# Kernel tuning notes

Hardware: AMD Instinct MI355X
Metric: run time of the kernel (lower is better)

## Reference

```python
import jax, jax.numpy as jnp
import numpy as np
import math

# Module config (matches init_kwargs)
FILTERS = 128
OUT_FACTOR = 0.5
B, H, W, C = 64, 64, 64, 64
HC = int(math.ceil(H / 2))  # weight/crop height = 32
WC = int(math.ceil(W / 2))  # weight/crop width  = 32
R_MIN = int(math.ceil(H * (1 - OUT_FACTOR) / 2))  # 16
R_MAX = R_MIN + int(math.ceil(H * (1 - OUT_FACTOR)))  # 48
C_MIN = int(math.ceil(W * (1 - OUT_FACTOR) / 2))  # 16
C_MAX = C_MIN + int(math.ceil(W * (1 - OUT_FACTOR)))  # 48


def setup_inputs() -> dict:
    key = jax.random.key(0)
    k1, k2, k3 = jax.random.split(key, 3)
    x = jax.random.normal(k1, (B, 2, H, W, C), dtype=jnp.float32)
    # keras 'random_normal' initializer: stddev 0.05
    W_r = jax.random.normal(k2, (HC, WC, C, FILTERS), dtype=jnp.float32) * 0.05
    W_i = jax.random.normal(k3, (HC, WC, C, FILTERS), dtype=jnp.float32) * 0.05
    b_r = jnp.zeros((FILTERS,), dtype=jnp.float32)
    b_i = jnp.zeros((FILTERS,), dtype=jnp.float32)
    return {"x": x, "W_r": W_r, "W_i": W_i, "b_r": b_r, "b_i": b_i}


def reference(x, W_r, W_i, b_r, b_i):
    # Crop center region: (B, 2, HC, WC, C)
    sp = x[:, :, R_MIN:R_MAX, C_MIN:C_MAX, :]
    xr, xi = sp[:, 0], sp[:, 1]  # (B, HC, WC, C)
    # Locally-connected complex contraction over channels (per-pixel weights)
    rr = jnp.einsum('bhwc,hwcf->bhwf', xr, W_r)
    ii = jnp.einsum('bhwc,hwcf->bhwf', xi, W_i)
    ri = jnp.einsum('bhwc,hwcf->bhwf', xr, W_i)
    ir = jnp.einsum('bhwc,hwcf->bhwf', xi, W_r)
    r = rr - ii + b_r  # (B, HC, WC, F)
    i = ri + ir + b_i
    y = jnp.stack([r, i], axis=1)  # (B, 2, HC, WC, F)
    # CReLU: relu applied independently to real and imaginary parts
    return jax.nn.relu(y)
```

## Files before the change

kernel.cpp:

```cpp
#include <hip/hip_runtime.h>

typedef __attribute__((ext_vector_type(8))) short short8;
typedef __attribute__((ext_vector_type(4))) float f32x4;
typedef __attribute__((ext_vector_type(4))) unsigned u32x4;

#define XSTR 72

__device__ __forceinline__ unsigned f2bf(float f) {
    unsigned u = __float_as_uint(f);
    return (u + 0x7fffu + ((u >> 16) & 1u)) >> 16;
}
__device__ __forceinline__ unsigned pack2(float lo, float hi) {
    return f2bf(lo) | (f2bf(hi) << 16);
}

__global__ __launch_bounds__(256, 4) void cplx_dot_kernel(
    const float* __restrict__ x, const float* __restrict__ Wr,
    const float* __restrict__ Wi, const float* __restrict__ br,
    const float* __restrict__ bi, float* __restrict__ out)
{
    __shared__ __align__(16) short sWr[128 * XSTR];
    __shared__ __align__(16) short sWi[128 * XSTR];

    const int bid = blockIdx.x;
    const int h = bid >> 5, w = bid & 31;
    const int t = threadIdx.x;
    const int wv = t >> 6, l = t & 63;
    const int lr = l & 15, lh = l >> 4;

    const int brow = 16 * wv + lr;
    const size_t gx = ((((size_t)brow * 2) * 64 + (16 + h)) * 64 + (16 + w)) * 64;
    const size_t gimg = (size_t)64 * 64 * 64;

    f32x4 vr[2][2], vi[2][2];
    #pragma unroll
    for (int kk = 0; kk < 2; ++kk) {
        const int c0 = 32 * kk + 8 * lh;
        vr[kk][0] = *(const f32x4*)(x + gx + c0);
        vr[kk][1] = *(const f32x4*)(x + gx + c0 + 4);
        vi[kk][0] = *(const f32x4*)(x + gx + gimg + c0);
        vi[kk][1] = *(const f32x4*)(x + gx + gimg + c0 + 4);
    }
    u32x4 ar[2], ai[2];
    #pragma unroll
    for (int kk = 0; kk < 2; ++kk) {
        #pragma unroll
        for (int p = 0; p < 2; ++p) {
            ar[kk][2 * p]     = pack2(vr[kk][p][0], vr[kk][p][1]);
            ar[kk][2 * p + 1] = pack2(vr[kk][p][2], vr[kk][p][3]);
            ai[kk][2 * p]     = pack2(vi[kk][p][0], vi[kk][p][1]);
            ai[kk][2 * p + 1] = pack2(vi[kk][p][2], vi[kk][p][3]);
        }
    }

    {
        const int g = t & 31, cg = t >> 5;
        const size_t wbase = (((size_t)h * 32 + w) * 64) * 128;
        f32x4 rr[8], ri[8];
        #pragma unroll
        for (int i = 0; i < 8; ++i) {
            size_t off = wbase + (size_t)(8 * cg + i) * 128 + 4 * g;
            rr[i] = *(const f32x4*)(Wr + off);
            ri[i] = *(const f32x4*)(Wi + off);
        }
        #pragma unroll
        for (int j = 0; j < 4; ++j) {
            u32x4 pr, pi;
            pr[0] = pack2(rr[0][j], rr[1][j]); pr[1] = pack2(rr[2][j], rr[3][j]);
            pr[2] = pack2(rr[4][j], rr[5][j]); pr[3] = pack2(rr[6][j], rr[7][j]);
            pi[0] = pack2(ri[0][j], ri[1][j]); pi[1] = pack2(ri[2][j], ri[3][j]);
            pi[2] = pack2(ri[4][j], ri[5][j]); pi[3] = pack2(ri[6][j], ri[7][j]);
            *(u32x4*)&sWr[(4 * g + j) * XSTR + 8 * cg] = pr;
            *(u32x4*)&sWi[(4 * g + j) * XSTR + 8 * cg] = pi;
        }
    }
    __syncthreads();

    f32x4 accR[8], accI[8];
    #pragma unroll
    for (int ft = 0; ft < 8; ++ft) {
        #pragma unroll
        for (int j = 0; j < 4; ++j) { accR[ft][j] = 0.f; accI[ft][j] = 0.f; }
    }

    #pragma unroll
    for (int kk = 0; kk < 2; ++kk) {
        const int c0 = 32 * kk + 8 * lh;
        short8 arf = __builtin_bit_cast(short8, ar[kk]);
        short8 aif = __builtin_bit_cast(short8, ai[kk]);
        short8 anf;
        #pragma unroll
        for (int j = 0; j < 8; ++j) anf[j] = aif[j] ^ (short)0x8000;
        #pragma unroll
        for (int ft = 0; ft < 8; ++ft) {
            short8 wr_ = *(const short8*)&sWr[(16 * ft + lr) * XSTR + c0];
            short8 wi_ = *(const short8*)&sWi[(16 * ft + lr) * XSTR + c0];
            accR[ft] = __builtin_amdgcn_mfma_f32_16x16x32_bf16(arf, wr_, accR[ft], 0, 0, 0);
            accR[ft] = __builtin_amdgcn_mfma_f32_16x16x32_bf16(anf, wi_, accR[ft], 0, 0, 0);
            accI[ft] = __builtin_amdgcn_mfma_f32_16x16x32_bf16(arf, wi_, accI[ft], 0, 0, 0);
            accI[ft] = __builtin_amdgcn_mfma_f32_16x16x32_bf16(aif, wr_, accI[ft], 0, 0, 0);
        }
    }

    #pragma unroll
    for (int ft = 0; ft < 8; ++ft) {
        const int fc = 16 * ft + lr;
        const float vbr = br[fc], vbi = bi[fc];
        #pragma unroll
        for (int j = 0; j < 4; ++j) {
            const int b = 16 * wv + 4 * lh + j;
            size_t o = ((((size_t)b * 2) * 32 + h) * 32 + w) * 128 + fc;
            out[o] = fmaxf(accR[ft][j] + vbr, 0.f);
            out[o + (size_t)32 * 32 * 128] = fmaxf(accI[ft][j] + vbi, 0.f);
        }
    }
}

extern "C" void kernel_launch(void* const* d_in, const int* in_sizes, int n_in,
                              void* d_out, int out_size, void* d_ws, size_t ws_size,
                              hipStream_t stream) {
    const float* x  = (const float*)d_in[0];
    const float* Wr = (const float*)d_in[1];
    const float* Wi = (const float*)d_in[2];
    const float* br = (const float*)d_in[3];
    const float* bi = (const float*)d_in[4];
    float* out = (float*)d_out;
    hipLaunchKernelGGL(cplx_dot_kernel, dim3(1024), dim3(256), 0, stream,
                       x, Wr, Wi, br, bi, out);
}
```

Before: 30.70 us.

## Process two pixels per block with double-buffered weight staging and prefetch

Each block now handles two adjacent w positions. It prefetches the second pixel's x and weight data from global memory while the first pixel's MFMA work and stores run, using two LDS buffers. The grid is halved to 512 blocks and launch bounds are lowered to 2 blocks per SM. This is meant to hide global load latency behind compute, at the cost of more registers, double the LDS, and fewer blocks for the GPU's many CUs.

```diff
diff --git a/kernel.cpp b/kernel.cpp
--- a/kernel.cpp
+++ b/kernel.cpp
@@ -14,25 +14,12 @@
     return f2bf(lo) | (f2bf(hi) << 16);
 }
 
-__global__ __launch_bounds__(256, 4) void cplx_dot_kernel(
-    const float* __restrict__ x, const float* __restrict__ Wr,
-    const float* __restrict__ Wi, const float* __restrict__ br,
-    const float* __restrict__ bi, float* __restrict__ out)
-{
-    __shared__ __align__(16) short sWr[128 * XSTR];
-    __shared__ __align__(16) short sWi[128 * XSTR];
 
-    const int bid = blockIdx.x;
-    const int h = bid >> 5, w = bid & 31;
-    const int t = threadIdx.x;
-    const int wv = t >> 6, l = t & 63;
-    const int lr = l & 15, lh = l >> 4;
-
-    const int brow = 16 * wv + lr;
+__device__ __forceinline__ void load_x(const float* __restrict__ x, int brow,
+                                       int h, int w, int lh,
+                                       f32x4 vr[2][2], f32x4 vi[2][2]) {
     const size_t gx = ((((size_t)brow * 2) * 64 + (16 + h)) * 64 + (16 + w)) * 64;
     const size_t gimg = (size_t)64 * 64 * 64;
-
-    f32x4 vr[2][2], vi[2][2];
     #pragma unroll
     for (int kk = 0; kk < 2; ++kk) {
         const int c0 = 32 * kk + 8 * lh;
@@ -41,9 +28,12 @@
         vi[kk][0] = *(const f32x4*)(x + gx + gimg + c0);
         vi[kk][1] = *(const f32x4*)(x + gx + gimg + c0 + 4);
     }
-    u32x4 ar[2], ai[2];
+}
+
+__device__ __forceinline__ void pack_x(const f32x4 vr[2][2], const f32x4 vi[2][2],
+                                       u32x4 ar[2], u32x4 ai[2]) {
     #pragma unroll
-    for (int kk = 0; kk < 2; ++kk) {
+    for (int kk = 0; kk < 2; ++kk)
         #pragma unroll
         for (int p = 0; p < 2; ++p) {
             ar[kk][2 * p]     = pack2(vr[kk][p][0], vr[kk][p][1]);
@@ -51,38 +41,45 @@
             ai[kk][2 * p]     = pack2(vi[kk][p][0], vi[kk][p][1]);
             ai[kk][2 * p + 1] = pack2(vi[kk][p][2], vi[kk][p][3]);
         }
+}
+
+__device__ __forceinline__ void load_W(const float* __restrict__ Wr,
+                                       const float* __restrict__ Wi,
+                                       int h, int w, int g, int cg,
+                                       f32x4 rr[8], f32x4 ri[8]) {
+    const size_t wbase = (((size_t)h * 32 + w) * 64) * 128;
+    #pragma unroll
+    for (int i = 0; i < 8; ++i) {
+        size_t off = wbase + (size_t)(8 * cg + i) * 128 + 4 * g;
+        rr[i] = *(const f32x4*)(Wr + off);
+        ri[i] = *(const f32x4*)(Wi + off);
     }
+}
 
-    {
-        const int g = t & 31, cg = t >> 5;
-        const size_t wbase = (((size_t)h * 32 + w) * 64) * 128;
-        f32x4 rr[8], ri[8];
-        #pragma unroll
-        for (int i = 0; i < 8; ++i) {
-            size_t off = wbase + (size_t)(8 * cg + i) * 128 + 4 * g;
-            rr[i] = *(const f32x4*)(Wr + off);
-            ri[i] = *(const f32x4*)(Wi + off);
-        }
-        #pragma unroll
-        for (int j = 0; j < 4; ++j) {
-            u32x4 pr, pi;
-            pr[0] = pack2(rr[0][j], rr[1][j]); pr[1] = pack2(rr[2][j], rr[3][j]);
-            pr[2] = pack2(rr[4][j], rr[5][j]); pr[3] = pack2(rr[6][j], rr[7][j]);
-            pi[0] = pack2(ri[0][j], ri[1][j]); pi[1] = pack2(ri[2][j], ri[3][j]);
-            pi[2] = pack2(ri[4][j], ri[5][j]); pi[3] = pack2(ri[6][j], ri[7][j]);
-            *(u32x4*)&sWr[(4 * g + j) * XSTR + 8 * cg] = pr;
-            *(u32x4*)&sWi[(4 * g + j) * XSTR + 8 * cg] = pi;
-        }
+__device__ __forceinline__ void pack_W(short* __restrict__ sWr, short* __restrict__ sWi,
+                                       int g, int cg,
+                                       const f32x4 rr[8], const f32x4 ri[8]) {
+    #pragma unroll
+    for (int j = 0; j < 4; ++j) {
+        u32x4 pr, pi;
+        pr[0] = pack2(rr[0][j], rr[1][j]); pr[1] = pack2(rr[2][j], rr[3][j]);
+        pr[2] = pack2(rr[4][j], rr[5][j]); pr[3] = pack2(rr[6][j], rr[7][j]);
+        pi[0] = pack2(ri[0][j], ri[1][j]); pi[1] = pack2(ri[2][j], ri[3][j]);
+        pi[2] = pack2(ri[4][j], ri[5][j]); pi[3] = pack2(ri[6][j], ri[7][j]);
+        *(u32x4*)&sWr[(4 * g + j) * XSTR + 8 * cg] = pr;
+        *(u32x4*)&sWi[(4 * g + j) * XSTR + 8 * cg] = pi;
     }
-    __syncthreads();
+}
 
-    f32x4 accR[8], accI[8];
+__device__ __forceinline__ void compute(const short* __restrict__ sWr,
+                                        const short* __restrict__ sWi,
+                                        const u32x4 ar[2], const u32x4 ai[2],
+                                        int lr, int lh,
+                                        f32x4 accR[8], f32x4 accI[8]) {
     #pragma unroll
-    for (int ft = 0; ft < 8; ++ft) {
+    for (int ft = 0; ft < 8; ++ft)
         #pragma unroll
         for (int j = 0; j < 4; ++j) { accR[ft][j] = 0.f; accI[ft][j] = 0.f; }
-    }
-
     #pragma unroll
     for (int kk = 0; kk < 2; ++kk) {
         const int c0 = 32 * kk + 8 * lh;
@@ -101,19 +98,70 @@
             accI[ft] = __builtin_amdgcn_mfma_f32_16x16x32_bf16(aif, wr_, accI[ft], 0, 0, 0);
         }
     }
+}
 
+__device__ __forceinline__ void store_out(float* __restrict__ out,
+                                          const f32x4 accR[8], const f32x4 accI[8],
+                                          const float vbr[8], const float vbi[8],
+                                          int h, int w, int wv, int lr, int lh) {
     #pragma unroll
     for (int ft = 0; ft < 8; ++ft) {
         const int fc = 16 * ft + lr;
-        const float vbr = br[fc], vbi = bi[fc];
         #pragma unroll
         for (int j = 0; j < 4; ++j) {
             const int b = 16 * wv + 4 * lh + j;
             size_t o = ((((size_t)b * 2) * 32 + h) * 32 + w) * 128 + fc;
-            out[o] = fmaxf(accR[ft][j] + vbr, 0.f);
-            out[o + (size_t)32 * 32 * 128] = fmaxf(accI[ft][j] + vbi, 0.f);
+            out[o] = fmaxf(accR[ft][j] + vbr[ft], 0.f);
+            out[o + (size_t)32 * 32 * 128] = fmaxf(accI[ft][j] + vbi[ft], 0.f);
         }
     }
+}
+
+__global__ __launch_bounds__(256, 2) void cplx_dot_kernel(
+    const float* __restrict__ x, const float* __restrict__ Wr,
+    const float* __restrict__ Wi, const float* __restrict__ br,
+    const float* __restrict__ bi, float* __restrict__ out)
+{
+    __shared__ __align__(16) short sW[2][2][128 * XSTR];
+
+    const int bid = blockIdx.x;
+    const int h = bid >> 4, qw = bid & 15;
+    const int w0 = 2 * qw, w1 = 2 * qw + 1;
+    const int t = threadIdx.x;
+    const int wv = t >> 6, l = t & 63;
+    const int lr = l & 15, lh = l >> 4;
+    const int g = t & 31, cg = t >> 5;
+    const int brow = 16 * wv + lr;
+
+    float vbr[8], vbi[8];
+    #pragma unroll
+    for (int ft = 0; ft < 8; ++ft) { vbr[ft] = br[16 * ft + lr]; vbi[ft] = bi[16 * ft + lr]; }
+
+    f32x4 xr0[2][2], xi0[2][2];
+    load_x(x, brow, h, w0, lh, xr0, xi0);
+    f32x4 wr0[8], wi0[8];
+    load_W(Wr, Wi, h, w0, g, cg, wr0, wi0);
+    pack_W(&sW[0][0][0], &sW[0][1][0], g, cg, wr0, wi0);
+    u32x4 ar0[2], ai0[2];
+    pack_x(xr0, xi0, ar0, ai0);
+    __syncthreads();
+
+    f32x4 xr1[2][2], xi1[2][2];
+    load_x(x, brow, h, w1, lh, xr1, xi1);
+    f32x4 wr1[8], wi1[8];
+    load_W(Wr, Wi, h, w1, g, cg, wr1, wi1);
+
+    f32x4 accR[8], accI[8];
+    compute(&sW[0][0][0], &sW[0][1][0], ar0, ai0, lr, lh, accR, accI);
+    store_out(out, accR, accI, vbr, vbi, h, w0, wv, lr, lh);
+
+    pack_W(&sW[1][0][0], &sW[1][1][0], g, cg, wr1, wi1);
+    u32x4 ar1[2], ai1[2];
+    pack_x(xr1, xi1, ar1, ai1);
+    __syncthreads();
+
+    compute(&sW[1][0][0], &sW[1][1][0], ar1, ai1, lr, lh, accR, accI);
+    store_out(out, accR, accI, vbr, vbi, h, w1, wv, lr, lh);
 }
 
 extern "C" void kernel_launch(void* const* d_in, const int* in_sizes, int n_in,
@@ -125,6 +173,6 @@
     const float* br = (const float*)d_in[3];
     const float* bi = (const float*)d_in[4];
     float* out = (float*)d_out;
-    hipLaunchKernelGGL(cplx_dot_kernel, dim3(1024), dim3(256), 0, stream,
+    hipLaunchKernelGGL(cplx_dot_kernel, dim3(512), dim3(256), 0, stream,
                        x, Wr, Wi, br, bi, out);
 }
```

Result: slower. 31.64 us (+3.1%).

## Switch to 32x32x16 MFMA tiles with wave split over batch and filter halves

Applied to the files above, without the earlier changes.

Replaces the 16x16x32 bf16 MFMA tiling, where each wave handled 16 batch rows across all 128 filters, with 32x32x16 MFMAs. Each wave now covers 32 batch rows by 64 filters, so each wave reads half as much weight data from LDS. Output stores become nontemporal and the occupancy hint drops from 4 to 3 blocks per CU. The x operand conversion moves after the weight staging, and the accumulators are consumed per filter tile, which may lower register pressure but changes the order of the output writes.

```diff
diff --git a/kernel.cpp b/kernel.cpp
--- a/kernel.cpp
+++ b/kernel.cpp
@@ -2,6 +2,7 @@
 
 typedef __attribute__((ext_vector_type(8))) short short8;
 typedef __attribute__((ext_vector_type(4))) float f32x4;
+typedef __attribute__((ext_vector_type(16))) float f32x16;
 typedef __attribute__((ext_vector_type(4))) unsigned u32x4;
 
 #define XSTR 72
@@ -14,7 +15,7 @@
     return f2bf(lo) | (f2bf(hi) << 16);
 }
 
-__global__ __launch_bounds__(256, 4) void cplx_dot_kernel(
+__global__ __launch_bounds__(256, 3) void cplx_dot_kernel(
     const float* __restrict__ x, const float* __restrict__ Wr,
     const float* __restrict__ Wi, const float* __restrict__ br,
     const float* __restrict__ bi, float* __restrict__ out)
@@ -26,31 +27,22 @@
     const int h = bid >> 5, w = bid & 31;
     const int t = threadIdx.x;
     const int wv = t >> 6, l = t & 63;
-    const int lr = l & 15, lh = l >> 4;
+    const int m = l & 31, kb = l >> 5;
+    const int mt = wv >> 1, fhalf = wv & 1;
 
-    const int brow = 16 * wv + lr;
+    const size_t gimg = (size_t)64 * 64 * 64;
+    const size_t oimg = (size_t)32 * 32 * 128;
+
+    const int brow = 32 * mt + m;
     const size_t gx = ((((size_t)brow * 2) * 64 + (16 + h)) * 64 + (16 + w)) * 64;
-    const size_t gimg = (size_t)64 * 64 * 64;
-
-    f32x4 vr[2][2], vi[2][2];
+    f32x4 vr[4][2], vi[4][2];
     #pragma unroll
-    for (int kk = 0; kk < 2; ++kk) {
-        const int c0 = 32 * kk + 8 * lh;
+    for (int kk = 0; kk < 4; ++kk) {
+        const int c0 = 16 * kk + 8 * kb;
         vr[kk][0] = *(const f32x4*)(x + gx + c0);
         vr[kk][1] = *(const f32x4*)(x + gx + c0 + 4);
         vi[kk][0] = *(const f32x4*)(x + gx + gimg + c0);
         vi[kk][1] = *(const f32x4*)(x + gx + gimg + c0 + 4);
-    }
-    u32x4 ar[2], ai[2];
-    #pragma unroll
-    for (int kk = 0; kk < 2; ++kk) {
-        #pragma unroll
-        for (int p = 0; p < 2; ++p) {
-            ar[kk][2 * p]     = pack2(vr[kk][p][0], vr[kk][p][1]);
-            ar[kk][2 * p + 1] = pack2(vr[kk][p][2], vr[kk][p][3]);
-            ai[kk][2 * p]     = pack2(vi[kk][p][0], vi[kk][p][1]);
-            ai[kk][2 * p + 1] = pack2(vi[kk][p][2], vi[kk][p][3]);
-        }
     }
 
     {
@@ -74,44 +66,47 @@
             *(u32x4*)&sWi[(4 * g + j) * XSTR + 8 * cg] = pi;
         }
     }
+
+    short8 ar[4], ai[4], an[4];
+    #pragma unroll
+    for (int kk = 0; kk < 4; ++kk) {
+        u32x4 pr, pi;
+        #pragma unroll
+        for (int p = 0; p < 2; ++p) {
+            pr[2 * p]     = pack2(vr[kk][p][0], vr[kk][p][1]);
+            pr[2 * p + 1] = pack2(vr[kk][p][2], vr[kk][p][3]);
+            pi[2 * p]     = pack2(vi[kk][p][0], vi[kk][p][1]);
+            pi[2 * p + 1] = pack2(vi[kk][p][2], vi[kk][p][3]);
+        }
+        ar[kk] = __builtin_bit_cast(short8, pr);
+        ai[kk] = __builtin_bit_cast(short8, pi);
+        #pragma unroll
+        for (int j = 0; j < 8; ++j) an[kk][j] = ai[kk][j] ^ (short)0x8000;
+    }
     __syncthreads();
 
-    f32x4 accR[8], accI[8];
     #pragma unroll
-    for (int ft = 0; ft < 8; ++ft) {
+    for (int ft = 0; ft < 2; ++ft) {
+        const int f = 64 * fhalf + 32 * ft + m;
+        f32x16 accR = {}, accI = {};
         #pragma unroll
-        for (int j = 0; j < 4; ++j) { accR[ft][j] = 0.f; accI[ft][j] = 0.f; }
-    }
-
-    #pragma unroll
-    for (int kk = 0; kk < 2; ++kk) {
-        const int c0 = 32 * kk + 8 * lh;
-        short8 arf = __builtin_bit_cast(short8, ar[kk]);
-        short8 aif = __builtin_bit_cast(short8, ai[kk]);
-        short8 anf;
+        for (int kk = 0; kk < 4; ++kk) {
+            const int c0 = 16 * kk + 8 * kb;
+            short8 wr_ = *(const short8*)&sWr[f * XSTR + c0];
+            short8 wi_ = *(const short8*)&sWi[f * XSTR + c0];
+            accR = __builtin_amdgcn_mfma_f32_32x32x16_bf16(ar[kk], wr_, accR, 0, 0, 0);
+            accR = __builtin_amdgcn_mfma_f32_32x32x16_bf16(an[kk], wi_, accR, 0, 0, 0);
+            accI = __builtin_amdgcn_mfma_f32_32x32x16_bf16(ar[kk], wi_, accI, 0, 0, 0);
+            accI = __builtin_amdgcn_mfma_f32_32x32x16_bf16(ai[kk], wr_, accI, 0, 0, 0);
+        }
+        const float bR = br[f], bI = bi[f];
         #pragma unroll
-        for (int j = 0; j < 8; ++j) anf[j] = aif[j] ^ (short)0x8000;
-        #pragma unroll
-        for (int ft = 0; ft < 8; ++ft) {
-            short8 wr_ = *(const short8*)&sWr[(16 * ft + lr) * XSTR + c0];
-            short8 wi_ = *(const short8*)&sWi[(16 * ft + lr) * XSTR + c0];
-            accR[ft] = __builtin_amdgcn_mfma_f32_16x16x32_bf16(arf, wr_, accR[ft], 0, 0, 0);
-            accR[ft] = __builtin_amdgcn_mfma_f32_16x16x32_bf16(anf, wi_, accR[ft], 0, 0, 0);
-            accI[ft] = __builtin_amdgcn_mfma_f32_16x16x32_bf16(arf, wi_, accI[ft], 0, 0, 0);
-            accI[ft] = __builtin_amdgcn_mfma_f32_16x16x32_bf16(aif, wr_, accI[ft], 0, 0, 0);
-        }
-    }
-
-    #pragma unroll
-    for (int ft = 0; ft < 8; ++ft) {
-        const int fc = 16 * ft + lr;
-        const float vbr = br[fc], vbi = bi[fc];
-        #pragma unroll
-        for (int j = 0; j < 4; ++j) {
-            const int b = 16 * wv + 4 * lh + j;
-            size_t o = ((((size_t)b * 2) * 32 + h) * 32 + w) * 128 + fc;
-            out[o] = fmaxf(accR[ft][j] + vbr, 0.f);
-            out[o + (size_t)32 * 32 * 128] = fmaxf(accI[ft][j] + vbi, 0.f);
+        for (int r = 0; r < 16; ++r) {
+            const int row = (r & 3) + 8 * (r >> 2) + 4 * kb;
+            const int b = 32 * mt + row;
+            size_t o = ((((size_t)b * 2) * 32 + h) * 32 + w) * 128 + f;
+            __builtin_nontemporal_store(fmaxf(accR[r] + bR, 0.f), out + o);
+            __builtin_nontemporal_store(fmaxf(accI[r] + bI, 0.f), out + o + oimg);
         }
     }
 }
```

Result: slower. 33.18 us (+8.1%).

## Split weight staging into two channel halves overlapping MFMA with conversion

Applied to the files above, without the earlier changes.

Loads all weights up front, then converts and stages only the first 32 input channels to shared memory, runs the first half of the MFMAs, and stages the second half before the remaining MFMAs. Output stores are interleaved with the second-half MFMA loop, and the __syncthreads calls are replaced with raw waitcnt/barrier asm. The aim is to overlap weight conversion and global stores with matrix compute in this memory-bound kernel. It lowers the occupancy hint from 4 to 3 blocks per CU to make room for the extra live registers. The second staging pass writes to shared memory with no barrier after the first-half reads, so a fast wave could overwrite values another wave is still reading, unless the row layout keeps the two halves apart.

```diff
diff --git a/kernel.cpp b/kernel.cpp
--- a/kernel.cpp
+++ b/kernel.cpp
@@ -2,6 +2,7 @@
 
 typedef __attribute__((ext_vector_type(8))) short short8;
 typedef __attribute__((ext_vector_type(4))) float f32x4;
+typedef __attribute__((ext_vector_type(2))) unsigned u32x2;
 typedef __attribute__((ext_vector_type(4))) unsigned u32x4;
 
 #define XSTR 72
@@ -14,7 +15,7 @@
     return f2bf(lo) | (f2bf(hi) << 16);
 }
 
-__global__ __launch_bounds__(256, 4) void cplx_dot_kernel(
+__global__ __launch_bounds__(256, 3) void cplx_dot_kernel(
     const float* __restrict__ x, const float* __restrict__ Wr,
     const float* __restrict__ Wi, const float* __restrict__ br,
     const float* __restrict__ bi, float* __restrict__ out)
@@ -27,11 +28,13 @@
     const int t = threadIdx.x;
     const int wv = t >> 6, l = t & 63;
     const int lr = l & 15, lh = l >> 4;
+    const int g = t & 31, cg = t >> 5;
+
+    const size_t gimg = (size_t)64 * 64 * 64;
+    const size_t oimg = (size_t)32 * 32 * 128;
 
     const int brow = 16 * wv + lr;
     const size_t gx = ((((size_t)brow * 2) * 64 + (16 + h)) * 64 + (16 + w)) * 64;
-    const size_t gimg = (size_t)64 * 64 * 64;
-
     f32x4 vr[2][2], vi[2][2];
     #pragma unroll
     for (int kk = 0; kk < 2; ++kk) {
@@ -41,77 +44,107 @@
         vi[kk][0] = *(const f32x4*)(x + gx + gimg + c0);
         vi[kk][1] = *(const f32x4*)(x + gx + gimg + c0 + 4);
     }
-    u32x4 ar[2], ai[2];
+
+    const size_t wbase = (((size_t)h * 32 + w) * 64) * 128;
+    f32x4 rr0[4], ri0[4], rr1[4], ri1[4];
+    #pragma unroll
+    for (int i = 0; i < 4; ++i) {
+        size_t off = wbase + (size_t)(4 * cg + i) * 128 + 4 * g;
+        rr0[i] = *(const f32x4*)(Wr + off);
+        ri0[i] = *(const f32x4*)(Wi + off);
+    }
+    #pragma unroll
+    for (int i = 0; i < 4; ++i) {
+        size_t off = wbase + (size_t)(32 + 4 * cg + i) * 128 + 4 * g;
+        rr1[i] = *(const f32x4*)(Wr + off);
+        ri1[i] = *(const f32x4*)(Wi + off);
+    }
+
+    short8 ar[2], ai[2];
     #pragma unroll
     for (int kk = 0; kk < 2; ++kk) {
+        u32x4 pr, pi;
         #pragma unroll
         for (int p = 0; p < 2; ++p) {
-            ar[kk][2 * p]     = pack2(vr[kk][p][0], vr[kk][p][1]);
-            ar[kk][2 * p + 1] = pack2(vr[kk][p][2], vr[kk][p][3]);
-            ai[kk][2 * p]     = pack2(vi[kk][p][0], vi[kk][p][1]);
-            ai[kk][2 * p + 1] = pack2(vi[kk][p][2], vi[kk][p][3]);
+            pr[2 * p]     = pack2(vr[kk][p][0], vr[kk][p][1]);
+            pr[2 * p + 1] = pack2(vr[kk][p][2], vr[kk][p][3]);
+            pi[2 * p]     = pack2(vi[kk][p][0], vi[kk][p][1]);
+            pi[2 * p + 1] = pack2(vi[kk][p][2], vi[kk][p][3]);
         }
+        ar[kk] = __builtin_bit_cast(short8, pr);
+        ai[kk] = __builtin_bit_cast(short8, pi);
     }
 
-    {
-        const int g = t & 31, cg = t >> 5;
-        const size_t wbase = (((size_t)h * 32 + w) * 64) * 128;
-        f32x4 rr[8], ri[8];
-        #pragma unroll
-        for (int i = 0; i < 8; ++i) {
-            size_t off = wbase + (size_t)(8 * cg + i) * 128 + 4 * g;
-            rr[i] = *(const f32x4*)(Wr + off);
-            ri[i] = *(const f32x4*)(Wi + off);
-        }
-        #pragma unroll
-        for (int j = 0; j < 4; ++j) {
-            u32x4 pr, pi;
-            pr[0] = pack2(rr[0][j], rr[1][j]); pr[1] = pack2(rr[2][j], rr[3][j]);
-            pr[2] = pack2(rr[4][j], rr[5][j]); pr[3] = pack2(rr[6][j], rr[7][j]);
-            pi[0] = pack2(ri[0][j], ri[1][j]); pi[1] = pack2(ri[2][j], ri[3][j]);
-            pi[2] = pack2(ri[4][j], ri[5][j]); pi[3] = pack2(ri[6][j], ri[7][j]);
-            *(u32x4*)&sWr[(4 * g + j) * XSTR + 8 * cg] = pr;
-            *(u32x4*)&sWi[(4 * g + j) * XSTR + 8 * cg] = pi;
-        }
+    #pragma unroll
+    for (int j = 0; j < 4; ++j) {
+        u32x2 pr, pi;
+        pr[0] = pack2(rr0[0][j], rr0[1][j]); pr[1] = pack2(rr0[2][j], rr0[3][j]);
+        pi[0] = pack2(ri0[0][j], ri0[1][j]); pi[1] = pack2(ri0[2][j], ri0[3][j]);
+        *(u32x2*)&sWr[(4 * g + j) * XSTR + 4 * cg] = pr;
+        *(u32x2*)&sWi[(4 * g + j) * XSTR + 4 * cg] = pi;
     }
-    __syncthreads();
+
+    asm volatile("s_waitcnt lgkmcnt(0)\n\ts_barrier" ::: "memory");
 
     f32x4 accR[8], accI[8];
     #pragma unroll
-    for (int ft = 0; ft < 8; ++ft) {
+    for (int ft = 0; ft < 8; ++ft)
         #pragma unroll
         for (int j = 0; j < 4; ++j) { accR[ft][j] = 0.f; accI[ft][j] = 0.f; }
-    }
 
-    #pragma unroll
-    for (int kk = 0; kk < 2; ++kk) {
-        const int c0 = 32 * kk + 8 * lh;
-        short8 arf = __builtin_bit_cast(short8, ar[kk]);
-        short8 aif = __builtin_bit_cast(short8, ai[kk]);
-        short8 anf;
+    {
+        short8 an0;
         #pragma unroll
-        for (int j = 0; j < 8; ++j) anf[j] = aif[j] ^ (short)0x8000;
+        for (int j = 0; j < 8; ++j) an0[j] = ai[0][j] ^ (short)0x8000;
+        const int c0 = 8 * lh;
         #pragma unroll
         for (int ft = 0; ft < 8; ++ft) {
             short8 wr_ = *(const short8*)&sWr[(16 * ft + lr) * XSTR + c0];
             short8 wi_ = *(const short8*)&sWi[(16 * ft + lr) * XSTR + c0];
-            accR[ft] = __builtin_amdgcn_mfma_f32_16x16x32_bf16(arf, wr_, accR[ft], 0, 0, 0);
-            accR[ft] = __builtin_amdgcn_mfma_f32_16x16x32_bf16(anf, wi_, accR[ft], 0, 0, 0);
-            accI[ft] = __builtin_amdgcn_mfma_f32_16x16x32_bf16(arf, wi_, accI[ft], 0, 0, 0);
-            accI[ft] = __builtin_amdgcn_mfma_f32_16x16x32_bf16(aif, wr_, accI[ft], 0, 0, 0);
+            accR[ft] = __builtin_amdgcn_mfma_f32_16x16x32_bf16(ar[0], wr_, accR[ft], 0, 0, 0);
+            accR[ft] = __builtin_amdgcn_mfma_f32_16x16x32_bf16(an0,   wi_, accR[ft], 0, 0, 0);
+            accI[ft] = __builtin_amdgcn_mfma_f32_16x16x32_bf16(ar[0], wi_, accI[ft], 0, 0, 0);
+            accI[ft] = __builtin_amdgcn_mfma_f32_16x16x32_bf16(ai[0], wr_, accI[ft], 0, 0, 0);
         }
     }
 
     #pragma unroll
-    for (int ft = 0; ft < 8; ++ft) {
-        const int fc = 16 * ft + lr;
-        const float vbr = br[fc], vbi = bi[fc];
+    for (int j = 0; j < 4; ++j) {
+        u32x2 pr, pi;
+        pr[0] = pack2(rr1[0][j], rr1[1][j]); pr[1] = pack2(rr1[2][j], rr1[3][j]);
+        pi[0] = pack2(ri1[0][j], ri1[1][j]); pi[1] = pack2(ri1[2][j], ri1[3][j]);
+        *(u32x2*)&sWr[(4 * g + j) * XSTR + 32 + 4 * cg] = pr;
+        *(u32x2*)&sWi[(4 * g + j) * XSTR + 32 + 4 * cg] = pi;
+    }
+
+    asm volatile("s_waitcnt lgkmcnt(0)\n\ts_barrier" ::: "memory");
+
+    float vbr[8], vbi[8];
+    #pragma unroll
+    for (int ft = 0; ft < 8; ++ft) { vbr[ft] = br[16 * ft + lr]; vbi[ft] = bi[16 * ft + lr]; }
+
+    {
+        short8 an1;
         #pragma unroll
-        for (int j = 0; j < 4; ++j) {
-            const int b = 16 * wv + 4 * lh + j;
-            size_t o = ((((size_t)b * 2) * 32 + h) * 32 + w) * 128 + fc;
-            out[o] = fmaxf(accR[ft][j] + vbr, 0.f);
-            out[o + (size_t)32 * 32 * 128] = fmaxf(accI[ft][j] + vbi, 0.f);
+        for (int j = 0; j < 8; ++j) an1[j] = ai[1][j] ^ (short)0x8000;
+        const int c0 = 32 + 8 * lh;
+        #pragma unroll
+        for (int ft = 0; ft < 8; ++ft) {
+            short8 wr_ = *(const short8*)&sWr[(16 * ft + lr) * XSTR + c0];
+            short8 wi_ = *(const short8*)&sWi[(16 * ft + lr) * XSTR + c0];
+            accR[ft] = __builtin_amdgcn_mfma_f32_16x16x32_bf16(ar[1], wr_, accR[ft], 0, 0, 0);
+            accR[ft] = __builtin_amdgcn_mfma_f32_16x16x32_bf16(an1,   wi_, accR[ft], 0, 0, 0);
+            accI[ft] = __builtin_amdgcn_mfma_f32_16x16x32_bf16(ar[1], wi_, accI[ft], 0, 0, 0);
+            accI[ft] = __builtin_amdgcn_mfma_f32_16x16x32_bf16(ai[1], wr_, accI[ft], 0, 0, 0);
+
+            const int fc = 16 * ft + lr;
+            #pragma unroll
+            for (int j = 0; j < 4; ++j) {
+                const int b = 16 * wv + 4 * lh + j;
+                size_t o = ((((size_t)b * 2) * 32 + h) * 32 + w) * 128 + fc;
+                out[o]        = fmaxf(accR[ft][j] + vbr[ft], 0.f);
+                out[o + oimg] = fmaxf(accI[ft][j] + vbi[ft], 0.f);
+            }
         }
     }
 }
```

Result: no change. 30.69 us (-0.0%).
